# Optimization experiments

Measured on AMD Instinct MI355X. Metric: run time of the kernel, lower is better.

The kernel has to match this reference:

```python
import jax, jax.numpy as jnp
import numpy as np

jax.config.update("jax_enable_x64", True)  # faithful int64 LIF state, as in the torch module

NUM_INPUTS = 700
NUM_HIDDEN = 4096
NUM_OUTPUT = 20
N_STEPS = 1000
ALPHA_SHIFT = 4   # synaptic-current decay shift
BETA_SHIFT = 3    # membrane decay shift
THRESHOLD = 1
BW1 = 64
BW2 = 64


def _sat(x, bw):
    # Quantize.saturate + to_int: clamp to signed bw-bit range, cast to int64.
    lo = -(2 ** (bw - 1))
    hi = 2 ** (bw - 1) - 1
    if jnp.issubdtype(x.dtype, jnp.floating):
        # values here are far below 2**63, so the float clip/cast is exact
        return jnp.clip(x, float(lo), float(hi)).astype(jnp.int64)
    return jnp.clip(x, lo, hi)


def _decay(v, shift):
    # LIF.exp_decay: v - (v >> shift) with arithmetic right shift on int64
    return v - (v >> shift)


def setup_inputs() -> dict:
    key = jax.random.key(0)
    k1, k2, k3, k4 = jax.random.split(key, 4)
    input_spikes = jax.random.randint(k1, (N_STEPS, NUM_INPUTS), 0, 2, dtype=jnp.int64)
    w1 = jax.random.randint(k2, (NUM_HIDDEN, NUM_INPUTS), -8, 8, dtype=jnp.int64)
    v1 = jax.random.randint(k3, (NUM_HIDDEN, NUM_HIDDEN), -8, 8, dtype=jnp.int64)
    w2 = jax.random.randint(k4, (NUM_OUTPUT, NUM_HIDDEN), -8, 8, dtype=jnp.int64)
    return {"input_spikes": input_spikes, "w1": w1, "v1": v1, "w2": w2}


def reference(input_spikes, w1, v1, w2):
    w1f = w1.astype(jnp.float32)
    v1f = v1.astype(jnp.float32)
    w2f = w2.astype(jnp.float32)
    # feed-forward input currents for all timesteps at once: [T, H]
    in_all = _sat(jnp.einsum("hi,ti->th", w1f, input_spikes.astype(jnp.float32)), BW1)

    H = w1.shape[0]
    O = w2.shape[0]
    z = lambda n: jnp.zeros((n,), dtype=jnp.int64)
    # state: hidden spikes, hidden mem, hidden syn, readout mem, readout syn
    init = (z(H), z(H), z(H), z(O), z(O))

    def step(state, in_cur):
        h_out, h_mem, h_syn, r_mem, r_syn = state
        # recurrent feedback current from PREVIOUS step's hidden spikes
        fb = _sat(jnp.einsum("hk,k->h", v1f, h_out.astype(jnp.float32)), BW1)
        syn_curr = _sat(in_cur + fb, BW1)
        # hidden LIF: reset (by previous spike) -> threshold -> decay/integrate
        h_mem = jnp.where(h_out == 1, 0, h_mem)
        new_out = (h_mem - THRESHOLD > 0).astype(jnp.int64)
        new_mem = _decay(h_mem, BETA_SHIFT) + h_syn
        new_syn = _decay(h_syn, ALPHA_SHIFT) + syn_curr
        # readout LIF (no reset); records updated membrane
        ro_cur = _sat(jnp.einsum("oh,h->o", w2f, new_out.astype(jnp.float32)), BW2)
        new_rmem = _decay(r_mem, BETA_SHIFT) + r_syn
        new_rsyn = _decay(r_syn, ALPHA_SHIFT) + ro_cur
        return (new_out, new_mem, new_syn, new_rmem, new_rsyn), new_rmem

    _, rec = jax.lax.scan(step, init, in_all)  # rec: [T, O]
    return rec.T  # torch.stack(ro_mem_rec, dim=1) -> [num_output, n_steps]
```

## Files before the change

### kernel.cpp

```cpp
#include <hip/hip_runtime.h>

#define T_STEPS 1000
#define N_IN    700
#define N_HID   4096
#define N_OUT   20
#define NBLK    64
#define HPB     64

typedef unsigned int u32x4 __attribute__((ext_vector_type(4)));

__device__ __forceinline__ u32x4 load_rec_sync(const u32x4* p) {
    u32x4 r;
    asm volatile("global_load_dwordx4 %0, %1, off sc0 sc1\n\t"
                 "s_waitcnt vmcnt(0)"
                 : "=v"(r) : "v"(p) : "memory");
    return r;
}
__device__ __forceinline__ void store_rec(u32x4* p, u32x4 v) {
    asm volatile("global_store_dwordx4 %0, %1, off sc0 sc1"
                 :: "v"(p), "v"(v) : "memory");
}

__global__ __launch_bounds__(256) void k_transpose_i8(
    const int* __restrict__ in, signed char* __restrict__ out,
    int R, int C, int out_stride)
{
    __shared__ signed char tile[32][33];
    const int cx = blockIdx.x * 32;
    const int ry = blockIdx.y * 32;
    const int tx = threadIdx.x;
    const int ty = threadIdx.y;
#pragma unroll
    for (int r = 0; r < 4; ++r) {
        int row = ry + ty + r * 8;
        int col = cx + tx;
        if (row < R && col < C)
            tile[ty + r * 8][tx] = (signed char)in[(size_t)row * C + col];
    }
    __syncthreads();
#pragma unroll
    for (int r = 0; r < 4; ++r) {
        int c   = cx + ty + r * 8;
        int row = ry + tx;
        if (c < C && row < R)
            out[(size_t)c * out_stride + row] = tile[tx][ty + r * 8];
    }
}

__global__ __launch_bounds__(256) void k_prep_v1(
    const int* __restrict__ in, unsigned char* __restrict__ out)
{
    __shared__ unsigned char tile[32][33];
    const int kx = blockIdx.x * 32;
    const int hy = blockIdx.y * 32;
    const int tx = threadIdx.x;
    const int ty = threadIdx.y;
#pragma unroll
    for (int r = 0; r < 4; ++r) {
        int h = hy + ty + r * 8;
        tile[ty + r * 8][tx] = (unsigned char)(in[(size_t)h * N_HID + kx + tx] + 8);
    }
    __syncthreads();
    const size_t bofs = (size_t)(hy >> 6) * (N_HID * 64) + (hy & 32);
#pragma unroll
    for (int r = 0; r < 4; ++r) {
        int k = kx + ty + r * 8;
        out[bofs + ((size_t)k << 6) + tx] = tile[tx][ty + r * 8];
    }
}

__global__ __launch_bounds__(256) void k_inall(
    const signed char* __restrict__ w1t,
    const int* __restrict__ spk,
    short* __restrict__ in_all2)
{
    __shared__ int s_spk[16][N_IN];
    const int t0 = blockIdx.y * 16;
    const int tcnt = min(16, T_STEPS - t0);
    const int tid = threadIdx.x;
    for (int b = 0; b < tcnt; ++b)
        for (int i = tid; i < N_IN; i += 256)
            s_spk[b][i] = spk[(size_t)(t0 + b) * N_IN + i];
    __syncthreads();
    const int h = blockIdx.x * 256 + tid;
    int acc[16];
#pragma unroll
    for (int b = 0; b < 16; ++b) acc[b] = 0;
    for (int i = 0; i < N_IN; ++i) {
        int w = (int)w1t[(size_t)i * N_HID + h];
#pragma unroll
        for (int b = 0; b < 16; ++b) acc[b] += w * s_spk[b][i];
    }
    const size_t base = (size_t)(h >> 6) * (T_STEPS * 64) + (h & 63);
    for (int b = 0; b < tcnt; ++b)
        in_all2[base + (size_t)(t0 + b) * 64] = (short)acc[b];
}

__global__ __launch_bounds__(256) void k_main(
    const short* __restrict__ in_all2,
    const unsigned char* __restrict__ v1b,
    u32x4* __restrict__ pub)
{
    const int tid  = threadIdx.x;
    const int wave = tid >> 6;
    const int lane = tid & 63;
    const int bid  = blockIdx.x;

    __shared__ unsigned short s_list[4][1024];
    __shared__ u32x4 s_rec[2][NBLK];
    __shared__ unsigned int s_part[2][4][4][8];
    __shared__ int s_nw[2][4];

    int mm = 0, synv = 0, out_t = 0;

    const unsigned char* gbase = v1b + ((size_t)bid << 18) + ((lane & 3) << 4);
    const int slot    = lane >> 2;
    const int mb      = (wave << 4) | slot;
    const int frag_sh = (lane & 3) << 4;
    const int kbase   = (mb << 6) + frag_sh;
    const short* in_base = in_all2 + (size_t)bid * (T_STEPS * 64) + lane;

    if (tid == 0) { u32x4 v = {0u, 0u, 1u, 0u}; store_rec(pub + bid, v); }
    __syncthreads();

    for (int t = 0; t < T_STEPS; ++t) {
        const int cur = t & 1;
        int in_cur = 0;
        if (wave == 0) {
            int mem_t = (mm - (mm >> 3)) + synv;
            int mnext = out_t ? 0 : mem_t;
            int out_n = (mnext - 1 > 0) ? 1 : 0;
            unsigned long long om = __ballot(out_n);
            if (lane == 0) {
                u32x4 v = {(unsigned)om, (unsigned)(om >> 32), 1u, 0u};
                store_rec(pub + (size_t)(t + 1) * NBLK + bid, v);
            }
            in_cur = (int)in_base[t * 64];
            mm = mnext; out_t = out_n;
        }

        unsigned int frag = 0;
        if (t > 0) {
            u32x4 rec = s_rec[cur][mb];
            if (rec.z == 0u) {
                const u32x4* rp = pub + (size_t)(t - 1) * NBLK + mb;
                do { __builtin_amdgcn_s_sleep(1); rec = load_rec_sync(rp); }
                while (rec.z == 0u);
            }
            unsigned long long km = ((unsigned long long)rec.y << 32) |
                                     (unsigned long long)rec.x;
            frag = (unsigned int)((km >> frag_sh) & 0xFFFFull);
        }
        int cnt = __popc(frag);
        int inc = cnt;
#pragma unroll
        for (int d = 1; d < 64; d <<= 1) {
            int v = __shfl_up(inc, d);
            if (lane >= d) inc += v;
        }
        int p = inc - cnt;
        unsigned int m = frag;
        while (m) {
            s_list[wave][p++] = (unsigned short)(kbase + __builtin_ctz(m));
            m &= m - 1;
        }
        const int n_w = __shfl(inc, 63);
        if (lane == 0) s_nw[cur][wave] = n_w;

        if (wave == 0)
            __builtin_amdgcn_global_load_lds(
                (const void*)(pub + (size_t)t * NBLK + lane),
                (void*)&s_rec[cur ^ 1][0], 16, 0,  17);

        asm volatile("s_waitcnt lgkmcnt(0)" ::: "memory");

        unsigned int a0=0,a1=0,a2=0,a3=0,a4=0,a5=0,a6=0,a7=0;
#pragma unroll 8
        for (int j = slot; j < n_w; j += 16) {
            int k = s_list[wave][j];
            u32x4 v = *(const u32x4*)(gbase + ((size_t)k << 6));
            const unsigned int M = 0x00FF00FFu;
            a0 += v.x & M;  a1 += (v.x >> 8) & M;
            a2 += v.y & M;  a3 += (v.y >> 8) & M;
            a4 += v.z & M;  a5 += (v.z >> 8) & M;
            a6 += v.w & M;  a7 += (v.w >> 8) & M;
        }
#pragma unroll
        for (int s = 4; s <= 32; s <<= 1) {
            a0 += __shfl_xor(a0, s); a1 += __shfl_xor(a1, s);
            a2 += __shfl_xor(a2, s); a3 += __shfl_xor(a3, s);
            a4 += __shfl_xor(a4, s); a5 += __shfl_xor(a5, s);
            a6 += __shfl_xor(a6, s); a7 += __shfl_xor(a7, s);
        }
        if (lane < 4) {
            unsigned int* sp = s_part[cur][wave][lane];
            sp[0]=a0; sp[1]=a1; sp[2]=a2; sp[3]=a3;
            sp[4]=a4; sp[5]=a5; sp[6]=a6; sp[7]=a7;
        }
        __syncthreads();

        if (wave == 0) {
            const int n = s_nw[cur][0] + s_nw[cur][1] + s_nw[cur][2] + s_nw[cur][3];
            const int li = lane >> 4, b = lane & 15;
            const int c = ((b >> 2) << 1) | (b & 1);
            const int half = (b >> 1) & 1;
            unsigned int s = s_part[cur][0][li][c] + s_part[cur][1][li][c]
                           + s_part[cur][2][li][c] + s_part[cur][3][li][c];
            int fb = (int)((s >> (half << 4)) & 0xFFFFu) - 8 * n;
            synv = (synv - (synv >> 4)) + in_cur + fb;
        }
    }
}

__global__ __launch_bounds__(256) void k_rocur(
    const int* __restrict__ w2,
    const u32x4* __restrict__ pub,
    int* __restrict__ ro)
{
    const int t = blockIdx.x;
    const int tid = threadIdx.x;
    __shared__ unsigned short s_list[N_HID];
    __shared__ int s_red[32][8];
    __shared__ int s_n;
    if (tid < 64) {
        u32x4 rec = pub[(size_t)t * NBLK + tid];
        unsigned long long m = (unsigned long long)rec.x |
                               ((unsigned long long)rec.y << 32);
        int cnt = __popcll(m);
        int inc = cnt;
#pragma unroll
        for (int d = 1; d < 64; d <<= 1) {
            int v = __shfl_up(inc, d);
            if (tid >= d) inc += v;
        }
        int p = inc - cnt;
        while (m) {
            s_list[p++] = (unsigned short)((tid << 6) | __builtin_ctzll(m));
            m &= m - 1;
        }
        if (tid == 63) s_n = inc;
    }
    __syncthreads();
    const int n = s_n;
    const int o = tid >> 3;
    const int r = tid & 7;
    if (o < N_OUT) {
        int acc = 0;
        for (int j = r; j < n; j += 8) acc += w2[(size_t)o * N_HID + s_list[j]];
        s_red[o][r] = acc;
    }
    __syncthreads();
    if (tid < N_OUT) {
        int acc = 0;
#pragma unroll
        for (int q = 0; q < 8; ++q) acc += s_red[tid][q];
        ro[(size_t)t * N_OUT + tid] = acc;
    }
}

#define CH 250
__global__ __launch_bounds__(256) void k_scan(const int* __restrict__ ro,
                                              int* __restrict__ out)
{
    __shared__ int s_ro[CH * N_OUT];
    __shared__ int s_out[CH * N_OUT];
    const int tid = threadIdx.x;
    int rm = 0, rs = 0;
    for (int c = 0; c < T_STEPS / CH; ++c) {
        for (int i = tid; i < CH * N_OUT; i += 256)
            s_ro[i] = ro[c * CH * N_OUT + i];
        __syncthreads();
        if (tid < N_OUT) {
            for (int j = 0; j < CH; ++j) {
                rm = (rm - (rm >> 3)) + rs;
                rs = (rs - (rs >> 4)) + s_ro[j * N_OUT + tid];
                s_out[j * N_OUT + tid] = rm;
            }
        }
        __syncthreads();
        for (int i = tid; i < CH * N_OUT; i += 256) {
            int o = i / CH, j = i - o * CH;
            out[o * T_STEPS + c * CH + j] = s_out[j * N_OUT + o];
        }
        __syncthreads();
    }
}

extern "C" void kernel_launch(void* const* d_in, const int* in_sizes, int n_in,
                              void* d_out, int out_size, void* d_ws, size_t ws_size,
                              hipStream_t stream)
{
    const int* spk = (const int*)d_in[0];
    const int* w1  = (const int*)d_in[1];
    const int* v1  = (const int*)d_in[2];
    const int* w2  = (const int*)d_in[3];
    int* out = (int*)d_out;

    char* ws = (char*)d_ws;
    constexpr size_t SZ_PUB    = (size_t)(T_STEPS + 1) * NBLK * 16;
    constexpr size_t OFF_PUB   = 0;
    constexpr size_t OFF_INALL = OFF_PUB + SZ_PUB;
    constexpr size_t OFF_V1B   = OFF_INALL + 8192000;
    constexpr size_t OFF_W1T   = OFF_V1B + 16777216;
    constexpr size_t OFF_RO    = OFF_W1T + 2867200;

    u32x4*          pub    = (u32x4*)(ws + OFF_PUB);
    short*          in_all = (short*)(ws + OFF_INALL);
    unsigned char*  v1b    = (unsigned char*)(ws + OFF_V1B);
    signed char*    w1t    = (signed char*)(ws + OFF_W1T);
    int*            ro     = (int*)(ws + OFF_RO);

    hipMemsetAsync(pub, 0, SZ_PUB, stream);

    dim3 tb(32, 8);
    k_prep_v1<<<dim3(128, 128), tb, 0, stream>>>(v1, v1b);
    k_transpose_i8<<<dim3(22, 128), tb, 0, stream>>>(w1, w1t, N_HID, N_IN, N_HID);
    k_inall<<<dim3(16, 63), 256, 0, stream>>>(w1t, spk, in_all);

    k_main<<<dim3(NBLK), dim3(256), 0, stream>>>(in_all, v1b, pub);

    k_rocur<<<dim3(T_STEPS), 256, 0, stream>>>(w2, pub, ro);
    k_scan<<<1, 256, 0, stream>>>(ro, out);
}
```

Before: 1.594 ms.

## Replace LDS spike compaction with per-lane bitmask walk over source block

Removes the per-step prefix-scan compaction of active spike indices into shared memory. Each group of four lanes now owns one source block and iterates directly over that block's 64-bit spike mask, loading the matching weight rows, while the spike count is reduced alongside the partial sums. This drops the shuffle scan, the LDS list writes and an lgkmcnt wait from the serial per-step critical path. In exchange the work per lane depends on its own block's popcount, so load balance across lanes can be worse than with the evenly strided compacted list.

```diff
diff --git a/kernel.cpp b/kernel.cpp
--- a/kernel.cpp
+++ b/kernel.cpp
@@ -106,18 +106,15 @@
     const int lane = tid & 63;
     const int bid  = blockIdx.x;
 
-    __shared__ unsigned short s_list[4][1024];
     __shared__ u32x4 s_rec[2][NBLK];
     __shared__ unsigned int s_part[2][4][4][8];
     __shared__ int s_nw[2][4];
 
     int mm = 0, synv = 0, out_t = 0;
 
-    const unsigned char* gbase = v1b + ((size_t)bid << 18) + ((lane & 3) << 4);
-    const int slot    = lane >> 2;
-    const int mb      = (wave << 4) | slot;
-    const int frag_sh = (lane & 3) << 4;
-    const int kbase   = (mb << 6) + frag_sh;
+    const int mb = (wave << 4) | (lane >> 2);
+    const unsigned char* gslot =
+        v1b + ((size_t)bid << 18) + ((size_t)mb << 12) + ((lane & 3) << 4);
     const short* in_base = in_all2 + (size_t)bid * (T_STEPS * 64) + lane;
 
     if (tid == 0) { u32x4 v = {0u, 0u, 1u, 0u}; store_rec(pub + bid, v); }
@@ -137,9 +134,12 @@
             }
             in_cur = (int)in_base[t * 64];
             mm = mnext; out_t = out_n;
-        }
-
-        unsigned int frag = 0;
+            __builtin_amdgcn_global_load_lds(
+                (const void*)(pub + (size_t)t * NBLK + lane),
+                (void*)&s_rec[cur ^ 1][0], 16, 0,  17);
+        }
+
+        unsigned int mlo = 0, mhi = 0;
         if (t > 0) {
             u32x4 rec = s_rec[cur][mb];
             if (rec.z == 0u) {
@@ -147,43 +147,31 @@
                 do { __builtin_amdgcn_s_sleep(1); rec = load_rec_sync(rp); }
                 while (rec.z == 0u);
             }
-            unsigned long long km = ((unsigned long long)rec.y << 32) |
-                                     (unsigned long long)rec.x;
-            frag = (unsigned int)((km >> frag_sh) & 0xFFFFull);
-        }
-        int cnt = __popc(frag);
-        int inc = cnt;
-#pragma unroll
-        for (int d = 1; d < 64; d <<= 1) {
-            int v = __shfl_up(inc, d);
-            if (lane >= d) inc += v;
-        }
-        int p = inc - cnt;
-        unsigned int m = frag;
-        while (m) {
-            s_list[wave][p++] = (unsigned short)(kbase + __builtin_ctz(m));
-            m &= m - 1;
-        }
-        const int n_w = __shfl(inc, 63);
-        if (lane == 0) s_nw[cur][wave] = n_w;
-
-        if (wave == 0)
-            __builtin_amdgcn_global_load_lds(
-                (const void*)(pub + (size_t)t * NBLK + lane),
-                (void*)&s_rec[cur ^ 1][0], 16, 0,  17);
-
-        asm volatile("s_waitcnt lgkmcnt(0)" ::: "memory");
+            mlo = rec.x; mhi = rec.y;
+        }
+        int myc = __popc(mlo) + __popc(mhi);
 
         unsigned int a0=0,a1=0,a2=0,a3=0,a4=0,a5=0,a6=0,a7=0;
-#pragma unroll 8
-        for (int j = slot; j < n_w; j += 16) {
-            int k = s_list[wave][j];
-            u32x4 v = *(const u32x4*)(gbase + ((size_t)k << 6));
-            const unsigned int M = 0x00FF00FFu;
-            a0 += v.x & M;  a1 += (v.x >> 8) & M;
-            a2 += v.y & M;  a3 += (v.y >> 8) & M;
-            a4 += v.z & M;  a5 += (v.z >> 8) & M;
-            a6 += v.w & M;  a7 += (v.w >> 8) & M;
+        const unsigned int M = 0x00FF00FFu;
+        {
+            unsigned int m0 = mlo;
+            while (m0) {
+                int b = __builtin_ctz(m0); m0 &= m0 - 1;
+                u32x4 v = *(const u32x4*)(gslot + ((size_t)b << 6));
+                a0 += v.x & M;  a1 += (v.x >> 8) & M;
+                a2 += v.y & M;  a3 += (v.y >> 8) & M;
+                a4 += v.z & M;  a5 += (v.z >> 8) & M;
+                a6 += v.w & M;  a7 += (v.w >> 8) & M;
+            }
+            unsigned int m1 = mhi;
+            while (m1) {
+                int b = __builtin_ctz(m1); m1 &= m1 - 1;
+                u32x4 v = *(const u32x4*)(gslot + ((size_t)(b + 32) << 6));
+                a0 += v.x & M;  a1 += (v.x >> 8) & M;
+                a2 += v.y & M;  a3 += (v.y >> 8) & M;
+                a4 += v.z & M;  a5 += (v.z >> 8) & M;
+                a6 += v.w & M;  a7 += (v.w >> 8) & M;
+            }
         }
 #pragma unroll
         for (int s = 4; s <= 32; s <<= 1) {
@@ -191,7 +179,9 @@
             a2 += __shfl_xor(a2, s); a3 += __shfl_xor(a3, s);
             a4 += __shfl_xor(a4, s); a5 += __shfl_xor(a5, s);
             a6 += __shfl_xor(a6, s); a7 += __shfl_xor(a7, s);
-        }
+            myc += __shfl_xor(myc, s);
+        }
+        if (lane == 0) s_nw[cur][wave] = myc;
         if (lane < 4) {
             unsigned int* sp = s_part[cur][wave][lane];
             sp[0]=a0; sp[1]=a1; sp[2]=a2; sp[3]=a3;
```

After: 1.661 ms. 4.2% more time.
